# Kernel tuning notes

Hardware: AMD Instinct MI355X
Metric: run time of the kernel (lower is better)

## Reference

```python
import jax, jax.numpy as jnp
import numpy as np

EMBED_DIM = 1024
NUM_HEADS = 16
HEAD_DIM = EMBED_DIM // NUM_HEADS
SCALING = HEAD_DIM ** -0.5


def setup_inputs() -> dict:
    key = jax.random.key(0)
    ks = jax.random.split(key, 10)
    B, S, D = 2, 2048, EMBED_DIM
    lim = 1.0 / np.sqrt(D)  # torch Linear default init scale
    def lin(k):
        kw, kb = jax.random.split(k)
        W = jax.random.uniform(kw, (D, D), jnp.float32, -lim, lim)
        b = jax.random.uniform(kb, (D,), jnp.float32, -lim, lim)
        return W, b
    Wq, bq = lin(ks[0])
    Wk, bk = lin(ks[1])
    Wv, bv = lin(ks[2])
    Wo, bo = lin(ks[3])
    hidden_states = jax.random.normal(ks[4], (B, S, D), jnp.float32)
    attention_mask = jnp.ones((B, S), jnp.int32)  # unused by the module's forward
    return {"hidden_states": hidden_states, "attention_mask": attention_mask,
            "Wq": Wq, "bq": bq, "Wk": Wk, "bk": bk, "Wv": Wv, "bv": bv,
            "Wo": Wo, "bo": bo}


def reference(hidden_states, attention_mask, Wq, bq, Wk, bk, Wv, bv, Wo, bo):
    B, S, D = hidden_states.shape
    H, hd = NUM_HEADS, HEAD_DIM

    def split_heads(x):  # [B,S,D] -> [B,H,S,hd]
        return x.reshape(B, S, H, hd).transpose(0, 2, 1, 3)

    q = split_heads(hidden_states @ Wq.T + bq) * SCALING
    k = split_heads(hidden_states @ Wk.T + bk)
    v = split_heads(hidden_states @ Wv.T + bv)

    scores = jnp.einsum("bhqd,bhkd->bhqk", q, k)  # [B,H,S,S]
    mask_value = jnp.finfo(scores.dtype).min
    causal = jnp.triu(jnp.ones((S, S), bool), k=1)  # True above diagonal
    scores = jnp.where(causal, mask_value, scores)
    probs = jax.nn.softmax(scores, axis=-1)

    out = jnp.einsum("bhqk,bhkd->bhqd", probs, v)  # [B,H,S,hd]
    out = out.transpose(0, 2, 1, 3).reshape(B, S, D)
    return out @ Wo.T + bo
```

## Files before the change

### kernel.cpp

```cpp
#include <hip/hip_runtime.h>


typedef __bf16 bf16;
typedef __attribute__((ext_vector_type(8))) __bf16 bf16x8;
typedef __attribute__((ext_vector_type(4))) __bf16 bf16x4;
typedef __attribute__((ext_vector_type(4))) float f32x4;
typedef __attribute__((ext_vector_type(4))) unsigned int u32x4;

#define MFMA16(a, b, c) __builtin_amdgcn_mfma_f32_16x16x32_bf16((a), (b), (c), 0, 0, 0)

__device__ __forceinline__ void gl_lds16(const bf16* g, bf16* l) {
  __builtin_amdgcn_global_load_lds(
      (__attribute__((address_space(1))) void*)g,
      (__attribute__((address_space(3))) void*)l, 16, 0, 0);
}

__device__ __forceinline__ float exp2_raw(float x) {
  float r;
  asm("v_exp_f32 %0, %1" : "=v"(r) : "v"(x));
  return r;
}

__global__ __launch_bounds__(256) void cvt5(
    const float* __restrict__ x, const float* __restrict__ wq,
    const float* __restrict__ wk, const float* __restrict__ wv,
    const float* __restrict__ wo,
    bf16* __restrict__ xb, bf16* __restrict__ wqb, bf16* __restrict__ wkb,
    bf16* __restrict__ wvb, bf16* __restrict__ wob) {
  const int bx = blockIdx.x;
  const float* s;
  bf16* d;
  int base;
  if (bx < 4096)      { s = x;  d = xb;  base = bx; }
  else if (bx < 5120) { s = wq; d = wqb; base = bx - 4096; }
  else if (bx < 6144) { s = wk; d = wkb; base = bx - 5120; }
  else if (bx < 7168) { s = wv; d = wvb; base = bx - 6144; }
  else                { s = wo; d = wob; base = bx - 7168; }
  const int i = base * 1024 + threadIdx.x * 4;
  const float4 v = *(const float4*)(s + i);
  bf16x4 o;
  o[0] = (bf16)v.x; o[1] = (bf16)v.y; o[2] = (bf16)v.z; o[3] = (bf16)v.w;
  *(bf16x4*)(d + i) = o;
}

template <int BM, typename OutT>
__global__ __launch_bounds__(256, 2) void gemm_bt3(
    const bf16* __restrict__ A,
    const bf16* __restrict__ W0, const bf16* __restrict__ W1, const bf16* __restrict__ W2,
    const float* __restrict__ B0, const float* __restrict__ B1, const float* __restrict__ B2,
    OutT* __restrict__ O0, OutT* __restrict__ O1, OutT* __restrict__ O2,
    float s0, float s1, float s2, int K, int vt_which) {
  constexpr int WM = BM / 32;
  __shared__ bf16 As[BM * 64];
  __shared__ bf16 Bs[128 * 64];

  const int t = threadIdx.x;
  const int lane = t & 63;
  const int wv = t >> 6;
  const int wm = wv & 1, wn = wv >> 1;
  const int qd = lane >> 4, ln = lane & 15;

  const int which = blockIdx.x >> 3;
  const bf16* W = (which == 0) ? W0 : (which == 1) ? W1 : W2;
  const float* Bi = (which == 0) ? B0 : (which == 1) ? B1 : B2;
  OutT* O = (which == 0) ? O0 : (which == 1) ? O1 : O2;
  const float scale = (which == 0) ? s0 : (which == 1) ? s1 : s2;

  const int n0 = (blockIdx.x & 7) * 128;
  const int m0 = blockIdx.y * BM;

  f32x4 acc[WM][4] = {};

  for (int k0 = 0; k0 < K; k0 += 64) {
#pragma unroll
    for (int i = 0; i < BM / 32; ++i) {
      const int s = i * 256 + t;
      const int row = s >> 3;
      const int c = (s & 7) ^ (row & 7);
      gl_lds16(A + (size_t)(m0 + row) * K + k0 + c * 8, &As[s * 8]);
    }
#pragma unroll
    for (int i = 0; i < 4; ++i) {
      const int s = i * 256 + t;
      const int row = s >> 3;
      const int c = (s & 7) ^ (row & 7);
      gl_lds16(W + (size_t)(n0 + row) * K + k0 + c * 8, &Bs[s * 8]);
    }
    __syncthreads();

#pragma unroll
    for (int ks = 0; ks < 2; ++ks) {
      bf16x8 af[WM], bw[4];
#pragma unroll
      for (int i = 0; i < WM; ++i) {
        const int r = wm * (BM / 2) + i * 16 + ln;
        af[i] = *(const bf16x8*)&As[r * 64 + (((ks * 4 + qd) ^ (ln & 7)) << 3)];
      }
#pragma unroll
      for (int j = 0; j < 4; ++j) {
        const int r = wn * 64 + j * 16 + ln;
        bw[j] = *(const bf16x8*)&Bs[r * 64 + (((ks * 4 + qd) ^ (ln & 7)) << 3)];
      }
#pragma unroll
      for (int i = 0; i < WM; ++i)
#pragma unroll
        for (int j = 0; j < 4; ++j)
          acc[i][j] = MFMA16(af[i], bw[j], acc[i][j]);
    }
    __syncthreads();
  }

#pragma unroll
  for (int i = 0; i < WM; ++i) {
    const int row = m0 + wm * (BM / 2) + i * 16 + qd * 4;
#pragma unroll
    for (int j = 0; j < 4; ++j) {
      const int col = n0 + wn * 64 + j * 16 + ln;
      const float bias = Bi[col];
      if (which == vt_which) {
        const int bb = row >> 11, ss = row & 2047;
        const int hh = col >> 6, dd = col & 63;
        OutT* dst = O + ((size_t)((bb << 4) + hh) * 64 + dd) * 2048 + ss;
        if constexpr (sizeof(OutT) == 2) {
          bf16x4 pk;
#pragma unroll
          for (int r = 0; r < 4; ++r) pk[r] = (bf16)((acc[i][j][r] + bias) * scale);
          *(bf16x4*)dst = pk;
        } else {
#pragma unroll
          for (int r = 0; r < 4; ++r) dst[r] = (OutT)((acc[i][j][r] + bias) * scale);
        }
      } else {
#pragma unroll
        for (int r = 0; r < 4; ++r) {
          const float v = (acc[i][j][r] + bias) * scale;
          O[(size_t)(row + r) * 1024 + col] = (OutT)v;
        }
      }
    }
  }
}

__global__ __launch_bounds__(256, 4) void attn_causal(
    const bf16* __restrict__ Q, const bf16* __restrict__ Kg,
    const bf16* __restrict__ VT, bf16* __restrict__ Ob) {
  __shared__ bf16 Ks[2][64 * 64];
  __shared__ bf16 Vts[2][64 * 64];

  const int t = threadIdx.x;
  const int lane = t & 63;
  const int w = t >> 6;
  const int qd = lane >> 4, ln = lane & 15;

  const int blk = blockIdx.x;
  const int bh = blk & 31;
  const int g = blk >> 5;
  const int a = g & 7, b = g >> 3;
  const int tq = (b == 0) ? (31 - a) : (b == 1) ? (16 + a) : (b == 2) ? (15 - a) : a;
  const int bb = bh >> 4, h = bh & 15;
  const size_t rowbase = (size_t)bb * 2048;
  const bf16* vtb = VT + (size_t)bh * 64 * 2048;

  const int q0 = tq * 64;
  const int nj = tq + 1;

  auto stage = [&](int buf, int j) {
    const bf16* kp = Kg + (rowbase + j * 64) * 1024 + h * 64;
#pragma unroll
    for (int i = 0; i < 2; ++i) {
      const int s = i * 256 + t;
      const int kv = s >> 3;
      const int c = (s & 7) ^ (kv & 7);
      gl_lds16(kp + (size_t)kv * 1024 + c * 8, &Ks[buf][s * 8]);
    }
#pragma unroll
    for (int i = 0; i < 2; ++i) {
      const int s = i * 256 + t;
      const int d = s >> 3;
      const int c = (s & 7) ^ (d & 7);
      gl_lds16(vtb + (size_t)d * 2048 + j * 64 + c * 8, &Vts[buf][s * 8]);
    }
  };

  const bf16* qp = Q + (rowbase + q0 + w * 16) * 1024 + h * 64;
  bf16x8 qf[2];
#pragma unroll
  for (int ks = 0; ks < 2; ++ks)
    qf[ks] = *(const bf16x8*)(qp + (size_t)ln * 1024 + ks * 32 + qd * 8);

  float l_run = 0.f;
  f32x4 accO[4] = {};

  stage(0, 0);

#pragma unroll 1
  for (int j = 0; j < nj; ++j) {
    const int buf = j & 1;
    __syncthreads();
    if (j + 1 < nj) stage(buf ^ 1, j + 1);

    f32x4 accT[4] = {};
    __builtin_amdgcn_s_setprio(1);
#pragma unroll
    for (int ks = 0; ks < 2; ++ks) {
#pragma unroll
      for (int nt = 0; nt < 4; ++nt) {
        const bf16x8 bk = *(const bf16x8*)
            &Ks[buf][(nt * 16 + ln) * 64 + (((ks * 4 + qd) ^ (ln & 7)) << 3)];
        accT[nt] = MFMA16(bk, qf[ks], accT[nt]);
      }
    }
    __builtin_amdgcn_s_setprio(0);

    float p[4][4];
    if (j == nj - 1) {
      const int qg = q0 + w * 16 + ln;
#pragma unroll
      for (int nt = 0; nt < 4; ++nt)
#pragma unroll
        for (int r = 0; r < 4; ++r) {
          float pv = exp2_raw(accT[nt][r]);
          const int kv = j * 64 + nt * 16 + qd * 4 + r;
          if (kv > qg) pv = 0.f;
          p[nt][r] = pv;
          l_run += pv;
        }
    } else {
#pragma unroll
      for (int nt = 0; nt < 4; ++nt)
#pragma unroll
        for (int r = 0; r < 4; ++r) {
          const float pv = exp2_raw(accT[nt][r]);
          p[nt][r] = pv;
          l_run += pv;
        }
    }

    unsigned int wd[2][4];
#pragma unroll
    for (int kt = 0; kt < 2; ++kt) {
      unsigned int L0, H0, L1, H1;
      asm("v_cvt_pk_bf16_f32 %0, %1, %2" : "=v"(L0) : "v"(p[2 * kt][0]), "v"(p[2 * kt][1]));
      asm("v_cvt_pk_bf16_f32 %0, %1, %2" : "=v"(H0) : "v"(p[2 * kt][2]), "v"(p[2 * kt][3]));
      asm("v_cvt_pk_bf16_f32 %0, %1, %2" : "=v"(L1) : "v"(p[2 * kt + 1][0]), "v"(p[2 * kt + 1][1]));
      asm("v_cvt_pk_bf16_f32 %0, %1, %2" : "=v"(H1) : "v"(p[2 * kt + 1][2]), "v"(p[2 * kt + 1][3]));
      asm("v_permlane32_swap_b32 %0, %1" : "+v"(L0), "+v"(L1));
      asm("v_permlane16_swap_b32 %0, %1" : "+v"(L0), "+v"(L1));
      asm("v_permlane32_swap_b32 %0, %1" : "+v"(H0), "+v"(H1));
      asm("v_permlane16_swap_b32 %0, %1" : "+v"(H0), "+v"(H1));
      wd[kt][0] = L0; wd[kt][1] = H0; wd[kt][2] = L1; wd[kt][3] = H1;
    }

    __builtin_amdgcn_s_setprio(1);
#pragma unroll
    for (int kt = 0; kt < 2; ++kt) {
      const u32x4 uw = {wd[kt][0], wd[kt][1], wd[kt][2], wd[kt][3]};
      const bf16x8 pa = __builtin_bit_cast(bf16x8, uw);
#pragma unroll
      for (int nt = 0; nt < 4; ++nt) {
        const bf16x8 bv = *(const bf16x8*)
            &Vts[buf][(nt * 16 + ln) * 64 + (((kt * 4 + qd) ^ (ln & 7)) << 3)];
        accO[nt] = MFMA16(pa, bv, accO[nt]);
      }
    }
    __builtin_amdgcn_s_setprio(0);
  }

  float l = l_run;
  l += __shfl_xor(l, 16, 64);
  l += __shfl_xor(l, 32, 64);
  const float inv = 1.0f / l;

  bf16* op = Ob + (rowbase + q0 + w * 16) * 1024 + h * 64;
#pragma unroll
  for (int r = 0; r < 4; ++r) {
    const float inv_r = __shfl(inv, (lane >> 4) * 4 + r, 64);
#pragma unroll
    for (int nt = 0; nt < 4; ++nt)
      op[(size_t)(qd * 4 + r) * 1024 + nt * 16 + ln] = (bf16)(accO[nt][r] * inv_r);
  }
}

extern "C" void kernel_launch(void* const* d_in, const int* in_sizes, int n_in,
                              void* d_out, int out_size, void* d_ws, size_t ws_size,
                              hipStream_t stream) {
  const float* X  = (const float*)d_in[0];
  const float* Wq = (const float*)d_in[2];
  const float* bq = (const float*)d_in[3];
  const float* Wk = (const float*)d_in[4];
  const float* bk = (const float*)d_in[5];
  const float* Wv = (const float*)d_in[6];
  const float* bv = (const float*)d_in[7];
  const float* Wo = (const float*)d_in[8];
  const float* bo = (const float*)d_in[9];
  float* out = (float*)d_out;

  bf16* xb  = (bf16*)d_ws;
  bf16* wqb = xb  + (size_t)4096 * 1024;
  bf16* wkb = wqb + (size_t)1024 * 1024;
  bf16* wvb = wkb + (size_t)1024 * 1024;
  bf16* wob = wvb + (size_t)1024 * 1024;
  bf16* q   = wob + (size_t)1024 * 1024;
  bf16* k   = q   + (size_t)4096 * 1024;
  bf16* vt  = k   + (size_t)4096 * 1024;
  bf16* ao  = xb;

  const float scaling = 0.125f * 1.44269504088896f;

  dim3 blk(256);
  cvt5<<<dim3(8192), blk, 0, stream>>>(X, Wq, Wk, Wv, Wo, xb, wqb, wkb, wvb, wob);
  gemm_bt3<128, bf16><<<dim3(24, 32), blk, 0, stream>>>(
      xb, wqb, wkb, wvb, bq, bk, bv, q, k, vt, scaling, 1.f, 1.f, 1024, 2);
  attn_causal<<<dim3(1024), blk, 0, stream>>>(q, k, vt, ao);
  gemm_bt3<64, float><<<dim3(8, 64), blk, 0, stream>>>(
      ao, wob, wob, wob, bo, bo, bo, out, out, out, 1.f, 1.f, 1.f, 1024, -1);
}
```

Before: 174.5 us.

## Split attention work 2x2 across waves over query and key halves with LDS reduction

The four waves are regrouped into a 2x2 grid. Each wave now handles 32 query rows against 32 of the 64 keys in a tile, instead of 16 query rows against all 64 keys. Each K and V fragment read from LDS is reused across two query sub-tiles, which roughly halves LDS read traffic per MFMA. The cost is an end-of-kernel reduction through LDS, where the key-half-1 waves write partial outputs and row sums for the key-half-0 waves to add, plus more accumulator registers per thread.

```diff
diff --git a/kernel.cpp b/kernel.cpp
--- a/kernel.cpp
+++ b/kernel.cpp
@@ -150,6 +150,7 @@
   const int t = threadIdx.x;
   const int lane = t & 63;
   const int w = t >> 6;
+  const int qh = w & 1, kh = w >> 1;
   const int qd = lane >> 4, ln = lane & 15;
 
   const int blk = blockIdx.x;
@@ -182,14 +183,16 @@
     }
   };
 
-  const bf16* qp = Q + (rowbase + q0 + w * 16) * 1024 + h * 64;
-  bf16x8 qf[2];
-#pragma unroll
-  for (int ks = 0; ks < 2; ++ks)
-    qf[ks] = *(const bf16x8*)(qp + (size_t)ln * 1024 + ks * 32 + qd * 8);
-
-  float l_run = 0.f;
-  f32x4 accO[4] = {};
+  const bf16* qp = Q + (rowbase + q0 + qh * 32) * 1024 + h * 64;
+  bf16x8 qf[2][2];
+#pragma unroll
+  for (int m = 0; m < 2; ++m)
+#pragma unroll
+    for (int ks = 0; ks < 2; ++ks)
+      qf[m][ks] = *(const bf16x8*)(qp + (size_t)(m * 16 + ln) * 1024 + ks * 32 + qd * 8);
+
+  float l_run[2] = {0.f, 0.f};
+  f32x4 accO[2][4] = {};
 
   stage(0, 0);
 
@@ -199,85 +202,118 @@
     __syncthreads();
     if (j + 1 < nj) stage(buf ^ 1, j + 1);
 
-    f32x4 accT[4] = {};
+    f32x4 accT[2][2] = {};
     __builtin_amdgcn_s_setprio(1);
 #pragma unroll
     for (int ks = 0; ks < 2; ++ks) {
 #pragma unroll
-      for (int nt = 0; nt < 4; ++nt) {
+      for (int nt = 0; nt < 2; ++nt) {
         const bf16x8 bk = *(const bf16x8*)
-            &Ks[buf][(nt * 16 + ln) * 64 + (((ks * 4 + qd) ^ (ln & 7)) << 3)];
-        accT[nt] = MFMA16(bk, qf[ks], accT[nt]);
+            &Ks[buf][(kh * 32 + nt * 16 + ln) * 64 + (((ks * 4 + qd) ^ (ln & 7)) << 3)];
+#pragma unroll
+        for (int m = 0; m < 2; ++m)
+          accT[m][nt] = MFMA16(bk, qf[m][ks], accT[m][nt]);
       }
     }
     __builtin_amdgcn_s_setprio(0);
 
-    float p[4][4];
+    float p[2][2][4];
     if (j == nj - 1) {
-      const int qg = q0 + w * 16 + ln;
-#pragma unroll
-      for (int nt = 0; nt < 4; ++nt)
-#pragma unroll
-        for (int r = 0; r < 4; ++r) {
-          float pv = exp2_raw(accT[nt][r]);
-          const int kv = j * 64 + nt * 16 + qd * 4 + r;
-          if (kv > qg) pv = 0.f;
-          p[nt][r] = pv;
-          l_run += pv;
-        }
+#pragma unroll
+      for (int m = 0; m < 2; ++m) {
+        const int qg = q0 + qh * 32 + m * 16 + ln;
+#pragma unroll
+        for (int nt = 0; nt < 2; ++nt)
+#pragma unroll
+          for (int r = 0; r < 4; ++r) {
+            float pv = exp2_raw(accT[m][nt][r]);
+            const int kv = j * 64 + kh * 32 + nt * 16 + qd * 4 + r;
+            if (kv > qg) pv = 0.f;
+            p[m][nt][r] = pv;
+            l_run[m] += pv;
+          }
+      }
     } else {
 #pragma unroll
-      for (int nt = 0; nt < 4; ++nt)
-#pragma unroll
-        for (int r = 0; r < 4; ++r) {
-          const float pv = exp2_raw(accT[nt][r]);
-          p[nt][r] = pv;
-          l_run += pv;
-        }
-    }
-
-    unsigned int wd[2][4];
-#pragma unroll
-    for (int kt = 0; kt < 2; ++kt) {
+      for (int m = 0; m < 2; ++m)
+#pragma unroll
+        for (int nt = 0; nt < 2; ++nt)
+#pragma unroll
+          for (int r = 0; r < 4; ++r) {
+            const float pv = exp2_raw(accT[m][nt][r]);
+            p[m][nt][r] = pv;
+            l_run[m] += pv;
+          }
+    }
+
+    u32x4 wd[2];
+#pragma unroll
+    for (int m = 0; m < 2; ++m) {
       unsigned int L0, H0, L1, H1;
-      asm("v_cvt_pk_bf16_f32 %0, %1, %2" : "=v"(L0) : "v"(p[2 * kt][0]), "v"(p[2 * kt][1]));
-      asm("v_cvt_pk_bf16_f32 %0, %1, %2" : "=v"(H0) : "v"(p[2 * kt][2]), "v"(p[2 * kt][3]));
-      asm("v_cvt_pk_bf16_f32 %0, %1, %2" : "=v"(L1) : "v"(p[2 * kt + 1][0]), "v"(p[2 * kt + 1][1]));
-      asm("v_cvt_pk_bf16_f32 %0, %1, %2" : "=v"(H1) : "v"(p[2 * kt + 1][2]), "v"(p[2 * kt + 1][3]));
+      asm("v_cvt_pk_bf16_f32 %0, %1, %2" : "=v"(L0) : "v"(p[m][0][0]), "v"(p[m][0][1]));
+      asm("v_cvt_pk_bf16_f32 %0, %1, %2" : "=v"(H0) : "v"(p[m][0][2]), "v"(p[m][0][3]));
+      asm("v_cvt_pk_bf16_f32 %0, %1, %2" : "=v"(L1) : "v"(p[m][1][0]), "v"(p[m][1][1]));
+      asm("v_cvt_pk_bf16_f32 %0, %1, %2" : "=v"(H1) : "v"(p[m][1][2]), "v"(p[m][1][3]));
       asm("v_permlane32_swap_b32 %0, %1" : "+v"(L0), "+v"(L1));
       asm("v_permlane16_swap_b32 %0, %1" : "+v"(L0), "+v"(L1));
       asm("v_permlane32_swap_b32 %0, %1" : "+v"(H0), "+v"(H1));
       asm("v_permlane16_swap_b32 %0, %1" : "+v"(H0), "+v"(H1));
-      wd[kt][0] = L0; wd[kt][1] = H0; wd[kt][2] = L1; wd[kt][3] = H1;
+      wd[m][0] = L0; wd[m][1] = H0; wd[m][2] = L1; wd[m][3] = H1;
     }
 
     __builtin_amdgcn_s_setprio(1);
 #pragma unroll
-    for (int kt = 0; kt < 2; ++kt) {
-      const u32x4 uw = {wd[kt][0], wd[kt][1], wd[kt][2], wd[kt][3]};
-      const bf16x8 pa = __builtin_bit_cast(bf16x8, uw);
-#pragma unroll
-      for (int nt = 0; nt < 4; ++nt) {
-        const bf16x8 bv = *(const bf16x8*)
-            &Vts[buf][(nt * 16 + ln) * 64 + (((kt * 4 + qd) ^ (ln & 7)) << 3)];
-        accO[nt] = MFMA16(pa, bv, accO[nt]);
+    for (int nt = 0; nt < 4; ++nt) {
+      const bf16x8 bv = *(const bf16x8*)
+          &Vts[buf][(nt * 16 + ln) * 64 + (((kh * 4 + qd) ^ (ln & 7)) << 3)];
+#pragma unroll
+      for (int m = 0; m < 2; ++m) {
+        const bf16x8 pa = __builtin_bit_cast(bf16x8, wd[m]);
+        accO[m][nt] = MFMA16(pa, bv, accO[m][nt]);
       }
     }
     __builtin_amdgcn_s_setprio(0);
   }
 
-  float l = l_run;
-  l += __shfl_xor(l, 16, 64);
-  l += __shfl_xor(l, 32, 64);
-  const float inv = 1.0f / l;
-
-  bf16* op = Ob + (rowbase + q0 + w * 16) * 1024 + h * 64;
-#pragma unroll
-  for (int r = 0; r < 4; ++r) {
-    const float inv_r = __shfl(inv, (lane >> 4) * 4 + r, 64);
-#pragma unroll
-    for (int nt = 0; nt < 4; ++nt)
-      op[(size_t)(qd * 4 + r) * 1024 + nt * 16 + ln] = (bf16)(accO[nt][r] * inv_r);
+  float lv[2];
+#pragma unroll
+  for (int m = 0; m < 2; ++m) {
+    float l = l_run[m];
+    l += __shfl_xor(l, 16, 64);
+    l += __shfl_xor(l, 32, 64);
+    lv[m] = l;
+  }
+  __syncthreads();
+  float* redO = (float*)&Ks[0][0];
+  float* redL = (float*)&Vts[0][0];
+  if (kh == 1) {
+#pragma unroll
+    for (int m = 0; m < 2; ++m) {
+#pragma unroll
+      for (int nt = 0; nt < 4; ++nt)
+#pragma unroll
+        for (int r = 0; r < 4; ++r)
+          redO[(size_t)qh * 2048 + (m * 16 + nt * 4 + r) * 64 + lane] = accO[m][nt][r];
+      if (lane < 16) redL[qh * 32 + m * 16 + lane] = lv[m];
+    }
+  }
+  __syncthreads();
+  if (kh == 0) {
+    bf16* op = Ob + (rowbase + q0 + qh * 32) * 1024 + h * 64;
+#pragma unroll
+    for (int m = 0; m < 2; ++m) {
+      const float inv = 1.0f / (lv[m] + redL[qh * 32 + m * 16 + ln]);
+#pragma unroll
+      for (int r = 0; r < 4; ++r) {
+        const float inv_r = __shfl(inv, (lane >> 4) * 4 + r, 64);
+#pragma unroll
+        for (int nt = 0; nt < 4; ++nt) {
+          const float o = accO[m][nt][r] +
+              redO[(size_t)qh * 2048 + (m * 16 + nt * 4 + r) * 64 + lane];
+          op[(size_t)(m * 16 + qd * 4 + r) * 1024 + nt * 16 + ln] = (bf16)(o * inv_r);
+        }
+      }
+    }
   }
 }
 
```

After: 180.5 us. +3.5%, slower.

## Pair complementary causal query tiles in one 512-thread block sharing K/V loads

Applied to the files above, without the earlier changes.

Each attention block now runs 8 waves in two groups. Each group handles one of a pair of complementary query tiles (t and 31-t), so every block does a balanced amount of causal work. K/V tiles staged into LDS are shared by both groups, which halves the global K/V traffic and the number of blocks. The cost is that the group with the shorter tile sits idle at barriers during the later iterations, and the larger blocks may lower occupancy flexibility.

```diff
diff --git a/kernel.cpp b/kernel.cpp
--- a/kernel.cpp
+++ b/kernel.cpp
@@ -141,7 +141,7 @@
   }
 }
 
-__global__ __launch_bounds__(256, 4) void attn_causal(
+__global__ __launch_bounds__(512, 4) void attn_causal(
     const bf16* __restrict__ Q, const bf16* __restrict__ Kg,
     const bf16* __restrict__ VT, bf16* __restrict__ Ob) {
   __shared__ bf16 Ks[2][64 * 64];
@@ -150,39 +150,38 @@
   const int t = threadIdx.x;
   const int lane = t & 63;
   const int w = t >> 6;
+  const int grp = w >> 2;
+  const int wq = w & 3;
   const int qd = lane >> 4, ln = lane & 15;
 
   const int blk = blockIdx.x;
   const int bh = blk & 31;
   const int g = blk >> 5;
-  const int a = g & 7, b = g >> 3;
-  const int tq = (b == 0) ? (31 - a) : (b == 1) ? (16 + a) : (b == 2) ? (15 - a) : a;
+  const int tB = (g < 8) ? (31 - g) : (g + 8);
+  const int tA = 31 - tB;
+  const int myT = grp ? tB : tA;
   const int bb = bh >> 4, h = bh & 15;
   const size_t rowbase = (size_t)bb * 2048;
   const bf16* vtb = VT + (size_t)bh * 64 * 2048;
 
-  const int q0 = tq * 64;
-  const int nj = tq + 1;
+  const int q0 = myT * 64 + wq * 16;
+  const int nj = tB + 1;
 
   auto stage = [&](int buf, int j) {
     const bf16* kp = Kg + (rowbase + j * 64) * 1024 + h * 64;
-#pragma unroll
-    for (int i = 0; i < 2; ++i) {
-      const int s = i * 256 + t;
-      const int kv = s >> 3;
-      const int c = (s & 7) ^ (kv & 7);
-      gl_lds16(kp + (size_t)kv * 1024 + c * 8, &Ks[buf][s * 8]);
-    }
-#pragma unroll
-    for (int i = 0; i < 2; ++i) {
-      const int s = i * 256 + t;
-      const int d = s >> 3;
-      const int c = (s & 7) ^ (d & 7);
-      gl_lds16(vtb + (size_t)d * 2048 + j * 64 + c * 8, &Vts[buf][s * 8]);
+    {
+      const int kv = t >> 3;
+      const int c = (t & 7) ^ (kv & 7);
+      gl_lds16(kp + (size_t)kv * 1024 + c * 8, &Ks[buf][t * 8]);
+    }
+    {
+      const int d = t >> 3;
+      const int c = (t & 7) ^ (d & 7);
+      gl_lds16(vtb + (size_t)d * 2048 + j * 64 + c * 8, &Vts[buf][t * 8]);
     }
   };
 
-  const bf16* qp = Q + (rowbase + q0 + w * 16) * 1024 + h * 64;
+  const bf16* qp = Q + (rowbase + q0) * 1024 + h * 64;
   bf16x8 qf[2];
 #pragma unroll
   for (int ks = 0; ks < 2; ++ks)
@@ -199,71 +198,73 @@
     __syncthreads();
     if (j + 1 < nj) stage(buf ^ 1, j + 1);
 
-    f32x4 accT[4] = {};
-    __builtin_amdgcn_s_setprio(1);
-#pragma unroll
-    for (int ks = 0; ks < 2; ++ks) {
-#pragma unroll
-      for (int nt = 0; nt < 4; ++nt) {
-        const bf16x8 bk = *(const bf16x8*)
-            &Ks[buf][(nt * 16 + ln) * 64 + (((ks * 4 + qd) ^ (ln & 7)) << 3)];
-        accT[nt] = MFMA16(bk, qf[ks], accT[nt]);
-      }
-    }
-    __builtin_amdgcn_s_setprio(0);
-
-    float p[4][4];
-    if (j == nj - 1) {
-      const int qg = q0 + w * 16 + ln;
-#pragma unroll
-      for (int nt = 0; nt < 4; ++nt)
-#pragma unroll
-        for (int r = 0; r < 4; ++r) {
-          float pv = exp2_raw(accT[nt][r]);
-          const int kv = j * 64 + nt * 16 + qd * 4 + r;
-          if (kv > qg) pv = 0.f;
-          p[nt][r] = pv;
-          l_run += pv;
+    if (j <= myT) {
+      f32x4 accT[4] = {};
+      __builtin_amdgcn_s_setprio(1);
+#pragma unroll
+      for (int ks = 0; ks < 2; ++ks) {
+#pragma unroll
+        for (int nt = 0; nt < 4; ++nt) {
+          const bf16x8 bk = *(const bf16x8*)
+              &Ks[buf][(nt * 16 + ln) * 64 + (((ks * 4 + qd) ^ (ln & 7)) << 3)];
+          accT[nt] = MFMA16(bk, qf[ks], accT[nt]);
         }
-    } else {
-#pragma unroll
-      for (int nt = 0; nt < 4; ++nt)
-#pragma unroll
-        for (int r = 0; r < 4; ++r) {
-          const float pv = exp2_raw(accT[nt][r]);
-          p[nt][r] = pv;
-          l_run += pv;
+      }
+      __builtin_amdgcn_s_setprio(0);
+
+      float p[4][4];
+      if (j == myT) {
+        const int qg = q0 + ln;
+#pragma unroll
+        for (int nt = 0; nt < 4; ++nt)
+#pragma unroll
+          for (int r = 0; r < 4; ++r) {
+            float pv = exp2_raw(accT[nt][r]);
+            const int kv = j * 64 + nt * 16 + qd * 4 + r;
+            if (kv > qg) pv = 0.f;
+            p[nt][r] = pv;
+            l_run += pv;
+          }
+      } else {
+#pragma unroll
+        for (int nt = 0; nt < 4; ++nt)
+#pragma unroll
+          for (int r = 0; r < 4; ++r) {
+            const float pv = exp2_raw(accT[nt][r]);
+            p[nt][r] = pv;
+            l_run += pv;
+          }
+      }
+
+      unsigned int wd[2][4];
+#pragma unroll
+      for (int kt = 0; kt < 2; ++kt) {
+        unsigned int L0, H0, L1, H1;
+        asm("v_cvt_pk_bf16_f32 %0, %1, %2" : "=v"(L0) : "v"(p[2 * kt][0]), "v"(p[2 * kt][1]));
+        asm("v_cvt_pk_bf16_f32 %0, %1, %2" : "=v"(H0) : "v"(p[2 * kt][2]), "v"(p[2 * kt][3]));
+        asm("v_cvt_pk_bf16_f32 %0, %1, %2" : "=v"(L1) : "v"(p[2 * kt + 1][0]), "v"(p[2 * kt + 1][1]));
+        asm("v_cvt_pk_bf16_f32 %0, %1, %2" : "=v"(H1) : "v"(p[2 * kt + 1][2]), "v"(p[2 * kt + 1][3]));
+        asm("v_permlane32_swap_b32 %0, %1" : "+v"(L0), "+v"(L1));
+        asm("v_permlane16_swap_b32 %0, %1" : "+v"(L0), "+v"(L1));
+        asm("v_permlane32_swap_b32 %0, %1" : "+v"(H0), "+v"(H1));
+        asm("v_permlane16_swap_b32 %0, %1" : "+v"(H0), "+v"(H1));
+        wd[kt][0] = L0; wd[kt][1] = H0; wd[kt][2] = L1; wd[kt][3] = H1;
+      }
+
+      __builtin_amdgcn_s_setprio(1);
+#pragma unroll
+      for (int kt = 0; kt < 2; ++kt) {
+        const u32x4 uw = {wd[kt][0], wd[kt][1], wd[kt][2], wd[kt][3]};
+        const bf16x8 pa = __builtin_bit_cast(bf16x8, uw);
+#pragma unroll
+        for (int nt = 0; nt < 4; ++nt) {
+          const bf16x8 bv = *(const bf16x8*)
+              &Vts[buf][(nt * 16 + ln) * 64 + (((kt * 4 + qd) ^ (ln & 7)) << 3)];
+          accO[nt] = MFMA16(pa, bv, accO[nt]);
         }
-    }
-
-    unsigned int wd[2][4];
-#pragma unroll
-    for (int kt = 0; kt < 2; ++kt) {
-      unsigned int L0, H0, L1, H1;
-      asm("v_cvt_pk_bf16_f32 %0, %1, %2" : "=v"(L0) : "v"(p[2 * kt][0]), "v"(p[2 * kt][1]));
-      asm("v_cvt_pk_bf16_f32 %0, %1, %2" : "=v"(H0) : "v"(p[2 * kt][2]), "v"(p[2 * kt][3]));
-      asm("v_cvt_pk_bf16_f32 %0, %1, %2" : "=v"(L1) : "v"(p[2 * kt + 1][0]), "v"(p[2 * kt + 1][1]));
-      asm("v_cvt_pk_bf16_f32 %0, %1, %2" : "=v"(H1) : "v"(p[2 * kt + 1][2]), "v"(p[2 * kt + 1][3]));
-      asm("v_permlane32_swap_b32 %0, %1" : "+v"(L0), "+v"(L1));
-      asm("v_permlane16_swap_b32 %0, %1" : "+v"(L0), "+v"(L1));
-      asm("v_permlane32_swap_b32 %0, %1" : "+v"(H0), "+v"(H1));
-      asm("v_permlane16_swap_b32 %0, %1" : "+v"(H0), "+v"(H1));
-      wd[kt][0] = L0; wd[kt][1] = H0; wd[kt][2] = L1; wd[kt][3] = H1;
-    }
-
-    __builtin_amdgcn_s_setprio(1);
-#pragma unroll
-    for (int kt = 0; kt < 2; ++kt) {
-      const u32x4 uw = {wd[kt][0], wd[kt][1], wd[kt][2], wd[kt][3]};
-      const bf16x8 pa = __builtin_bit_cast(bf16x8, uw);
-#pragma unroll
-      for (int nt = 0; nt < 4; ++nt) {
-        const bf16x8 bv = *(const bf16x8*)
-            &Vts[buf][(nt * 16 + ln) * 64 + (((kt * 4 + qd) ^ (ln & 7)) << 3)];
-        accO[nt] = MFMA16(pa, bv, accO[nt]);
-      }
-    }
-    __builtin_amdgcn_s_setprio(0);
+      }
+      __builtin_amdgcn_s_setprio(0);
+    }
   }
 
   float l = l_run;
@@ -271,7 +272,7 @@
   l += __shfl_xor(l, 32, 64);
   const float inv = 1.0f / l;
 
-  bf16* op = Ob + (rowbase + q0 + w * 16) * 1024 + h * 64;
+  bf16* op = Ob + (rowbase + q0) * 1024 + h * 64;
 #pragma unroll
   for (int r = 0; r < 4; ++r) {
     const float inv_r = __shfl(inv, (lane >> 4) * 4 + r, 64);
@@ -311,7 +312,7 @@
   cvt5<<<dim3(8192), blk, 0, stream>>>(X, Wq, Wk, Wv, Wo, xb, wqb, wkb, wvb, wob);
   gemm_bt3<128, bf16><<<dim3(24, 32), blk, 0, stream>>>(
       xb, wqb, wkb, wvb, bq, bk, bv, q, k, vt, scaling, 1.f, 1.f, 1024, 2);
-  attn_causal<<<dim3(1024), blk, 0, stream>>>(q, k, vt, ao);
+  attn_causal<<<dim3(512), dim3(512), 0, stream>>>(q, k, vt, ao);
   gemm_bt3<64, float><<<dim3(8, 64), blk, 0, stream>>>(
       ao, wob, wob, wob, bo, bo, bo, out, out, out, 1.f, 1.f, 1.f, 1024, -1);
 }
```

Result: no change. 172.8 us (-1.0%).
